# Optimization experiments

Hardware: AMD Instinct MI355X
Metric: run time of the kernel (lower is better)

The kernel has to match this reference:

```python
import jax, jax.numpy as jnp
import numpy as np
import math

B, T = 32768, 34
VOCAB = 14
SQRT_HD = math.sqrt(3.0)

def _pos_flat_index():
    # flatten (source, index) pairs into indices of a [14,3] table:
    # rows 0-9 = digit spiral enc, row 10 = z10_enc, rows 11-13 = special_enc
    flat = []
    for p in range(34):
        if p < 10:
            flat.append(p)
        elif p == 10:
            flat.append(11 + 0)
        elif p < 21:
            flat.append(p - 11)
        elif p == 21:
            flat.append(11 + 1)
        elif p < 33:
            z = p - 22
            flat.append(z if z < 10 else 10)
        else:
            flat.append(11 + 2)
    return np.array(flat, dtype=np.int32)

POS_FLAT = _pos_flat_index()

def setup_inputs() -> dict:
    key = jax.random.key(0)
    ks = jax.random.split(key, 12)
    r = lambda k, s: jax.random.normal(k, s, dtype=jnp.float32)
    return {
        'idx': jax.random.randint(ks[0], (B, T), 0, VOCAB, dtype=jnp.int64),
        'tok_emb': r(ks[1], (14, 3)),
        'pos_params': r(ks[2], (4,)),
        'z10_enc': r(ks[3], (1, 3)),
        'special_enc': r(ks[4], (3, 3)),
        'wq': r(ks[5], (3, 6)), 'wk': r(ks[6], (3, 6)), 'wv': r(ks[7], (3, 6)),
        'wo': r(ks[8], (6, 6)),
        'ln1_g': jnp.ones(6), 'ln1_b': jnp.zeros(6),
        'ln2_g': jnp.ones(6), 'ln2_b': jnp.zeros(6),
        'lnf_g': jnp.ones(6), 'lnf_b': jnp.zeros(6),
        'ffn_w1': r(ks[9], (6, 2)), 'ffn_b1': jnp.zeros(2),
        'ffn_w2': r(ks[10], (2, 6)), 'ffn_b2': jnp.zeros(6),
        'head_w': r(ks[11], (6, 3)),
    }

def _ln(x, g, b):
    mu = x.mean(-1, keepdims=True)
    var = ((x - mu) ** 2).mean(-1, keepdims=True)
    return (x - mu) * jax.lax.rsqrt(var + 1e-5) * g + b

def _forward(idx, tok_emb, pos_params, z10_enc, special_enc, wq, wk, wv, wo,
             ln1_g, ln1_b, ln2_g, ln2_b, lnf_g, lnf_b,
             ffn_w1, ffn_b1, ffn_w2, ffn_b2, head_w):
    amp, phase, slope, offset = pos_params[0], pos_params[1], pos_params[2], pos_params[3]
    i = jnp.arange(10, dtype=jnp.float32)
    ang = 2.0 * math.pi * i / 10.0 + phase
    digit = jnp.stack([amp * jnp.cos(ang), amp * jnp.sin(ang), slope * i + offset], -1)  # [10,3]
    table = jnp.concatenate([digit, z10_enc, special_enc], 0)  # [14,3]
    Tn = idx.shape[1]
    pos = table[POS_FLAT][:Tn]  # [T,3]
    tok = tok_emb[idx]  # [B,T,3]
    x = jnp.concatenate([tok, jnp.broadcast_to(pos, tok.shape)], -1)  # [B,T,6]
    h = _ln(x, ln1_g, ln1_b)
    h_tok, h_pos = h[..., :3], h[..., 3:]
    Bn = idx.shape[0]
    q = (h_pos @ wq).reshape(Bn, Tn, 2, 3)
    k = (h_pos @ wk).reshape(Bn, Tn, 2, 3)
    v = (h_tok @ wv).reshape(Bn, Tn, 2, 3)
    attn = jnp.einsum('bqhd,bkhd->bhqk', q, k) / SQRT_HD
    mask = jnp.tril(jnp.ones((Tn, Tn), bool))
    attn = jax.nn.softmax(jnp.where(mask, attn, -jnp.inf), axis=-1)
    o = jnp.einsum('bhqk,bkhd->bqhd', attn, v).reshape(Bn, Tn, 6)
    x = x + o @ wo
    h2 = _ln(x, ln2_g, ln2_b)
    x = x + (jax.nn.gelu(h2 @ ffn_w1 + ffn_b1, approximate=False) @ ffn_w2 + ffn_b2)
    x = _ln(x, lnf_g, lnf_b)
    return (x @ head_w) @ tok_emb.T  # [B,T,14]

def reference(idx, tok_emb, pos_params, z10_enc, special_enc, wq, wk, wv, wo,
              ln1_g, ln1_b, ln2_g, ln2_b, lnf_g, lnf_b,
              ffn_w1, ffn_b1, ffn_w2, ffn_b2, head_w):
    return _forward(idx, tok_emb, pos_params, z10_enc, special_enc, wq, wk, wv, wo,
                    ln1_g, ln1_b, ln2_g, ln2_b, lnf_g, lnf_b,
                    ffn_w1, ffn_b1, ffn_w2, ffn_b2, head_w)
```

## Files before the change

### kernel.cpp

```cpp
#include <hip/hip_runtime.h>
#include <math.h>

#define BT    34
#define TPR   17
#define RPB   15
#define BLOCK 256

typedef float v4f __attribute__((ext_vector_type(4)));

__device__ __forceinline__ void ln6(const float* x, const float* g, const float* b, float* o) {
  float mu = (x[0]+x[1]+x[2]+x[3]+x[4]+x[5]) * (1.0f/6.0f);
  float v = 0.f;
  #pragma unroll
  for (int c = 0; c < 6; ++c) { float d = x[c]-mu; v += d*d; }
  float inv = rsqrtf(v * (1.0f/6.0f) + 1e-5f);
  #pragma unroll
  for (int c = 0; c < 6; ++c) o[c] = (x[c]-mu)*inv*g[c] + b[c];
}

__global__ __launch_bounds__(BLOCK, 4)
void addtrans_kernel(const int* __restrict__ idx,
                     const float* __restrict__ tok_emb,
                     const float* __restrict__ pos_params,
                     const float* __restrict__ z10_enc,
                     const float* __restrict__ special_enc,
                     const float* __restrict__ wq,
                     const float* __restrict__ wk,
                     const float* __restrict__ wv,
                     const float* __restrict__ wo,
                     const float* __restrict__ ln1_g, const float* __restrict__ ln1_b,
                     const float* __restrict__ ln2_g, const float* __restrict__ ln2_b,
                     const float* __restrict__ lnf_g, const float* __restrict__ lnf_b,
                     const float* __restrict__ ffn_w1, const float* __restrict__ ffn_b1,
                     const float* __restrict__ ffn_w2, const float* __restrict__ ffn_b2,
                     const float* __restrict__ head_w,
                     float* __restrict__ out, int B)
{
  __shared__ __align__(16) float s_mem[RPB*BT*14];
  __shared__ float s_te[42];
  __shared__ float s_pos[BT*3];
  __shared__ float s_wq[18], s_wk[18], s_wv[18], s_wo[36], s_hw[18];
  __shared__ float s_g1[6], s_b1[6], s_g2[6], s_b2[6], s_gf[6], s_bf[6];
  __shared__ float s_w1[12], s_w2[12], s_fb1[2], s_fb2[6];

  const int tid = threadIdx.x;

  if (tid < 42) s_te[tid] = tok_emb[tid];
  if (tid < 18) { s_wq[tid]=wq[tid]; s_wk[tid]=wk[tid]; s_wv[tid]=wv[tid]; s_hw[tid]=head_w[tid]; }
  if (tid < 36) s_wo[tid] = wo[tid];
  if (tid < 12) { s_w1[tid]=ffn_w1[tid]; s_w2[tid]=ffn_w2[tid]; }
  if (tid < 6)  { s_g1[tid]=ln1_g[tid]; s_b1[tid]=ln1_b[tid];
                  s_g2[tid]=ln2_g[tid]; s_b2[tid]=ln2_b[tid];
                  s_gf[tid]=lnf_g[tid]; s_bf[tid]=lnf_b[tid];
                  s_fb2[tid]=ffn_b2[tid]; }
  if (tid < 2)  s_fb1[tid] = ffn_b1[tid];
  if (tid < BT) {
    int p = tid, f;
    if (p < 10) f = p;
    else if (p == 10) f = 11;
    else if (p < 21) f = p - 11;
    else if (p == 21) f = 12;
    else if (p < 33) { int z = p - 22; f = (z < 10) ? z : 10; }
    else f = 13;
    float e0, e1, e2;
    if (f < 10) {
      float amp = pos_params[0], ph = pos_params[1], sl = pos_params[2], of = pos_params[3];
      float ang = 0.62831853071795864769f * (float)f + ph;
      e0 = amp * cosf(ang); e1 = amp * sinf(ang); e2 = sl * (float)f + of;
    } else if (f == 10) { e0 = z10_enc[0]; e1 = z10_enc[1]; e2 = z10_enc[2]; }
    else { int u = f - 11; e0 = special_enc[u*3]; e1 = special_enc[u*3+1]; e2 = special_enc[u*3+2]; }
    s_pos[tid*3+0] = e0; s_pos[tid*3+1] = e1; s_pos[tid*3+2] = e2;
  }
  __syncthreads();

  const int row = tid / TPR;
  const int j   = tid - row * TPR;
  const int b   = blockIdx.x * RPB + row;
  const bool active = (row < RPB) && (b < B);

  float q[2][6], xr[2][6];

  if (active) {
    const int base = b * BT;
    #pragma unroll
    for (int s = 0; s < 2; ++s) {
      const int t = j + s * TPR;
      const int vid = idx[base + t];
      float x6[6];
      x6[0] = s_te[vid*3+0]; x6[1] = s_te[vid*3+1]; x6[2] = s_te[vid*3+2];
      x6[3] = s_pos[t*3+0];  x6[4] = s_pos[t*3+1];  x6[5] = s_pos[t*3+2];
      float h[6];
      ln6(x6, s_g1, s_b1, h);
      float* kvp = &s_mem[(row*BT + t)*12];
      #pragma unroll
      for (int c = 0; c < 6; ++c) {
        q[s][c] = 0.57735026918962576451f *
                  (h[3]*s_wq[c] + h[4]*s_wq[6+c] + h[5]*s_wq[12+c]);
        kvp[c]   = h[3]*s_wk[c] + h[4]*s_wk[6+c] + h[5]*s_wk[12+c];
        kvp[6+c] = h[0]*s_wv[c] + h[1]*s_wv[6+c] + h[2]*s_wv[12+c];
        xr[s][c] = x6[c];
      }
    }
  }
  __syncthreads();

  float l[2][2] = {{0.f,0.f},{0.f,0.f}};
  float o[2][6] = {{0.f,0.f,0.f,0.f,0.f,0.f},{0.f,0.f,0.f,0.f,0.f,0.f}};
  if (active) {
    const float* kvb = &s_mem[row * (BT*12)];
    #pragma unroll 2
    for (int k = 0; k < TPR; ++k) {
      float4 A  = *(const float4*)(kvb + k*12 + 0);
      float4 Bv = *(const float4*)(kvb + k*12 + 4);
      float4 C  = *(const float4*)(kvb + k*12 + 8);
      float sa = q[0][0]*A.x + q[0][1]*A.y + q[0][2]*A.z;
      float sb = q[0][3]*A.w + q[0][4]*Bv.x + q[0][5]*Bv.y;
      float pa = __expf(sa), pb = __expf(sb);
      const bool m = (k <= j);
      pa = m ? pa : 0.f; pb = m ? pb : 0.f;
      l[0][0] += pa; l[0][1] += pb;
      o[0][0] += pa*Bv.z; o[0][1] += pa*Bv.w; o[0][2] += pa*C.x;
      o[0][3] += pb*C.y;  o[0][4] += pb*C.z;  o[0][5] += pb*C.w;
      float sc = q[1][0]*A.x + q[1][1]*A.y + q[1][2]*A.z;
      float sd = q[1][3]*A.w + q[1][4]*Bv.x + q[1][5]*Bv.y;
      float pc = __expf(sc), pd = __expf(sd);
      l[1][0] += pc; l[1][1] += pd;
      o[1][0] += pc*Bv.z; o[1][1] += pc*Bv.w; o[1][2] += pc*C.x;
      o[1][3] += pd*C.y;  o[1][4] += pd*C.z;  o[1][5] += pd*C.w;
    }
    #pragma unroll 2
    for (int k = TPR; k < BT; ++k) {
      float4 A  = *(const float4*)(kvb + k*12 + 0);
      float4 Bv = *(const float4*)(kvb + k*12 + 4);
      float4 C  = *(const float4*)(kvb + k*12 + 8);
      float sc = q[1][0]*A.x + q[1][1]*A.y + q[1][2]*A.z;
      float sd = q[1][3]*A.w + q[1][4]*Bv.x + q[1][5]*Bv.y;
      float pc = __expf(sc), pd = __expf(sd);
      const bool m = (k <= j + TPR);
      pc = m ? pc : 0.f; pd = m ? pd : 0.f;
      l[1][0] += pc; l[1][1] += pd;
      o[1][0] += pc*Bv.z; o[1][1] += pc*Bv.w; o[1][2] += pc*C.x;
      o[1][3] += pd*C.y;  o[1][4] += pd*C.z;  o[1][5] += pd*C.w;
    }
  }
  __syncthreads();

  if (active) {
    #pragma unroll
    for (int s = 0; s < 2; ++s) {
      const int t = j + s * TPR;
      const float ia = 1.0f / l[s][0], ib = 1.0f / l[s][1];
      float a6[6] = { o[s][0]*ia, o[s][1]*ia, o[s][2]*ia,
                      o[s][3]*ib, o[s][4]*ib, o[s][5]*ib };
      float xn[6];
      #pragma unroll
      for (int c = 0; c < 6; ++c) {
        xn[c] = xr[s][c]
              + a6[0]*s_wo[c]    + a6[1]*s_wo[6+c]  + a6[2]*s_wo[12+c]
              + a6[3]*s_wo[18+c] + a6[4]*s_wo[24+c] + a6[5]*s_wo[30+c];
      }
      float h2[6];
      ln6(xn, s_g2, s_b2, h2);
      float a0 = s_fb1[0], a1 = s_fb1[1];
      #pragma unroll
      for (int d = 0; d < 6; ++d) { a0 += h2[d]*s_w1[d*2]; a1 += h2[d]*s_w1[d*2+1]; }
      const float g0 = 0.5f*a0*(1.0f + erff(a0*0.70710678118654752440f));
      const float g1 = 0.5f*a1*(1.0f + erff(a1*0.70710678118654752440f));
      #pragma unroll
      for (int c = 0; c < 6; ++c) xn[c] += g0*s_w2[c] + g1*s_w2[6+c] + s_fb2[c];
      float xf[6];
      ln6(xn, s_gf, s_bf, xf);
      float y0 = 0.f, y1 = 0.f, y2 = 0.f;
      #pragma unroll
      for (int c = 0; c < 6; ++c) {
        y0 += xf[c]*s_hw[c*3+0]; y1 += xf[c]*s_hw[c*3+1]; y2 += xf[c]*s_hw[c*3+2];
      }
      float* lp = &s_mem[(row*BT + t)*14];
      #pragma unroll
      for (int j2 = 0; j2 < 14; ++j2)
        lp[j2] = y0*s_te[j2*3+0] + y1*s_te[j2*3+1] + y2*s_te[j2*3+2];
    }
  }
  __syncthreads();

  {
    const int b0 = blockIdx.x * RPB;
    int nrows = B - b0; if (nrows > RPB) nrows = RPB;
    if (nrows > 0) {
      const int n4 = nrows * (BT*14/4);
      v4f* dst = reinterpret_cast<v4f*>(out + (size_t)b0 * (BT*14));
      const v4f* src = reinterpret_cast<const v4f*>(s_mem);
      for (int i = tid; i < n4; i += BLOCK)
        __builtin_nontemporal_store(src[i], dst + i);
    }
  }
}

extern "C" void kernel_launch(void* const* d_in, const int* in_sizes, int n_in,
                              void* d_out, int out_size, void* d_ws, size_t ws_size,
                              hipStream_t stream) {
  const int B = in_sizes[0] / BT;
  const int grid = (B + RPB - 1) / RPB;
  addtrans_kernel<<<grid, BLOCK, 0, stream>>>(
      (const int*)d_in[0],   (const float*)d_in[1], (const float*)d_in[2],
      (const float*)d_in[3], (const float*)d_in[4], (const float*)d_in[5],
      (const float*)d_in[6], (const float*)d_in[7], (const float*)d_in[8],
      (const float*)d_in[9], (const float*)d_in[10], (const float*)d_in[11],
      (const float*)d_in[12], (const float*)d_in[13], (const float*)d_in[14],
      (const float*)d_in[15], (const float*)d_in[16], (const float*)d_in[17],
      (const float*)d_in[18], (const float*)d_in[19],
      (float*)d_out, B);
}
```

Before: 145.4 us.

## Pack attention math into float2 ops, use exp2, and store outputs directly

```diff
diff --git a/kernel.cpp b/kernel.cpp
--- a/kernel.cpp
+++ b/kernel.cpp
@@ -6,7 +6,16 @@
 #define RPB   15
 #define BLOCK 256
 
+typedef float v2f __attribute__((ext_vector_type(2)));
 typedef float v4f __attribute__((ext_vector_type(4)));
+
+#define QSCALE 0.83294037332470f
+
+#if __has_builtin(__builtin_amdgcn_exp2f)
+#define EXP2(x) __builtin_amdgcn_exp2f(x)
+#else
+#define EXP2(x) exp2f(x)
+#endif
 
 __device__ __forceinline__ void ln6(const float* x, const float* g, const float* b, float* o) {
   float mu = (x[0]+x[1]+x[2]+x[3]+x[4]+x[5]) * (1.0f/6.0f);
@@ -36,7 +45,7 @@
                      const float* __restrict__ head_w,
                      float* __restrict__ out, int B)
 {
-  __shared__ __align__(16) float s_mem[RPB*BT*14];
+  __shared__ __align__(16) float s_kv[RPB*BT*12];
   __shared__ float s_te[42];
   __shared__ float s_pos[BT*3];
   __shared__ float s_wq[18], s_wk[18], s_wv[18], s_wo[36], s_hw[18];
@@ -78,7 +87,8 @@
   const int b   = blockIdx.x * RPB + row;
   const bool active = (row < RPB) && (b < B);
 
-  float q[2][6], xr[2][6];
+  v2f   qp[2][3];
+  float xr[2][6];
 
   if (active) {
     const int base = b * BT;
@@ -91,67 +101,67 @@
       x6[3] = s_pos[t*3+0];  x6[4] = s_pos[t*3+1];  x6[5] = s_pos[t*3+2];
       float h[6];
       ln6(x6, s_g1, s_b1, h);
-      float* kvp = &s_mem[(row*BT + t)*12];
+      float q6[6], k6[6], v6[6];
       #pragma unroll
       for (int c = 0; c < 6; ++c) {
-        q[s][c] = 0.57735026918962576451f *
-                  (h[3]*s_wq[c] + h[4]*s_wq[6+c] + h[5]*s_wq[12+c]);
-        kvp[c]   = h[3]*s_wk[c] + h[4]*s_wk[6+c] + h[5]*s_wk[12+c];
-        kvp[6+c] = h[0]*s_wv[c] + h[1]*s_wv[6+c] + h[2]*s_wv[12+c];
+        q6[c] = h[3]*s_wq[c] + h[4]*s_wq[6+c] + h[5]*s_wq[12+c];
+        k6[c] = h[3]*s_wk[c] + h[4]*s_wk[6+c] + h[5]*s_wk[12+c];
+        v6[c] = h[0]*s_wv[c] + h[1]*s_wv[6+c] + h[2]*s_wv[12+c];
         xr[s][c] = x6[c];
       }
+      qp[s][0] = (v2f){q6[0]*QSCALE, q6[3]*QSCALE};
+      qp[s][1] = (v2f){q6[1]*QSCALE, q6[4]*QSCALE};
+      qp[s][2] = (v2f){q6[2]*QSCALE, q6[5]*QSCALE};
+      v4f* kvp = (v4f*)&s_kv[(row*BT + t)*12];
+      kvp[0] = (v4f){k6[0], k6[3], k6[1], k6[4]};
+      kvp[1] = (v4f){k6[2], k6[5], v6[0], v6[3]};
+      kvp[2] = (v4f){v6[1], v6[4], v6[2], v6[5]};
     }
   }
   __syncthreads();
 
-  float l[2][2] = {{0.f,0.f},{0.f,0.f}};
-  float o[2][6] = {{0.f,0.f,0.f,0.f,0.f,0.f},{0.f,0.f,0.f,0.f,0.f,0.f}};
+  v2f l0 = (v2f){0.f,0.f}, l1 = (v2f){0.f,0.f};
+  v2f o0[3] = {(v2f){0.f,0.f},(v2f){0.f,0.f},(v2f){0.f,0.f}};
+  v2f o1[3] = {(v2f){0.f,0.f},(v2f){0.f,0.f},(v2f){0.f,0.f}};
   if (active) {
-    const float* kvb = &s_mem[row * (BT*12)];
-    #pragma unroll 2
+    const v4f* kvb = (const v4f*)&s_kv[row * (BT*12)];
+    #pragma unroll 4
     for (int k = 0; k < TPR; ++k) {
-      float4 A  = *(const float4*)(kvb + k*12 + 0);
-      float4 Bv = *(const float4*)(kvb + k*12 + 4);
-      float4 C  = *(const float4*)(kvb + k*12 + 8);
-      float sa = q[0][0]*A.x + q[0][1]*A.y + q[0][2]*A.z;
-      float sb = q[0][3]*A.w + q[0][4]*Bv.x + q[0][5]*Bv.y;
-      float pa = __expf(sa), pb = __expf(sb);
-      const bool m = (k <= j);
-      pa = m ? pa : 0.f; pb = m ? pb : 0.f;
-      l[0][0] += pa; l[0][1] += pb;
-      o[0][0] += pa*Bv.z; o[0][1] += pa*Bv.w; o[0][2] += pa*C.x;
-      o[0][3] += pb*C.y;  o[0][4] += pb*C.z;  o[0][5] += pb*C.w;
-      float sc = q[1][0]*A.x + q[1][1]*A.y + q[1][2]*A.z;
-      float sd = q[1][3]*A.w + q[1][4]*Bv.x + q[1][5]*Bv.y;
-      float pc = __expf(sc), pd = __expf(sd);
-      l[1][0] += pc; l[1][1] += pd;
-      o[1][0] += pc*Bv.z; o[1][1] += pc*Bv.w; o[1][2] += pc*C.x;
-      o[1][3] += pd*C.y;  o[1][4] += pd*C.z;  o[1][5] += pd*C.w;
-    }
-    #pragma unroll 2
+      v4f A = kvb[k*3+0], Bv = kvb[k*3+1], C = kvb[k*3+2];
+      v2f kA = (v2f){A.x, A.y}, kB = (v2f){A.z, A.w}, kC = (v2f){Bv.x, Bv.y};
+      v2f vA = (v2f){Bv.z, Bv.w}, vB = (v2f){C.x, C.y}, vC = (v2f){C.z, C.w};
+      v2f s0 = qp[0][0]*kA + qp[0][1]*kB + qp[0][2]*kC;
+      const float mf = (k <= j) ? 1.f : 0.f;
+      v2f p0 = (v2f){EXP2(s0.x), EXP2(s0.y)};
+      p0 *= mf;
+      l0 += p0; o0[0] += p0*vA; o0[1] += p0*vB; o0[2] += p0*vC;
+      v2f s1 = qp[1][0]*kA + qp[1][1]*kB + qp[1][2]*kC;
+      v2f p1 = (v2f){EXP2(s1.x), EXP2(s1.y)};
+      l1 += p1; o1[0] += p1*vA; o1[1] += p1*vB; o1[2] += p1*vC;
+    }
+    #pragma unroll 4
     for (int k = TPR; k < BT; ++k) {
-      float4 A  = *(const float4*)(kvb + k*12 + 0);
-      float4 Bv = *(const float4*)(kvb + k*12 + 4);
-      float4 C  = *(const float4*)(kvb + k*12 + 8);
-      float sc = q[1][0]*A.x + q[1][1]*A.y + q[1][2]*A.z;
-      float sd = q[1][3]*A.w + q[1][4]*Bv.x + q[1][5]*Bv.y;
-      float pc = __expf(sc), pd = __expf(sd);
-      const bool m = (k <= j + TPR);
-      pc = m ? pc : 0.f; pd = m ? pd : 0.f;
-      l[1][0] += pc; l[1][1] += pd;
-      o[1][0] += pc*Bv.z; o[1][1] += pc*Bv.w; o[1][2] += pc*C.x;
-      o[1][3] += pd*C.y;  o[1][4] += pd*C.z;  o[1][5] += pd*C.w;
-    }
-  }
-  __syncthreads();
+      v4f A = kvb[k*3+0], Bv = kvb[k*3+1], C = kvb[k*3+2];
+      v2f kA = (v2f){A.x, A.y}, kB = (v2f){A.z, A.w}, kC = (v2f){Bv.x, Bv.y};
+      v2f vA = (v2f){Bv.z, Bv.w}, vB = (v2f){C.x, C.y}, vC = (v2f){C.z, C.w};
+      v2f s1 = qp[1][0]*kA + qp[1][1]*kB + qp[1][2]*kC;
+      const float mf = (k <= j + TPR) ? 1.f : 0.f;
+      v2f p1 = (v2f){EXP2(s1.x), EXP2(s1.y)};
+      p1 *= mf;
+      l1 += p1; o1[0] += p1*vA; o1[1] += p1*vB; o1[2] += p1*vC;
+    }
+  }
 
   if (active) {
     #pragma unroll
     for (int s = 0; s < 2; ++s) {
       const int t = j + s * TPR;
-      const float ia = 1.0f / l[s][0], ib = 1.0f / l[s][1];
-      float a6[6] = { o[s][0]*ia, o[s][1]*ia, o[s][2]*ia,
-                      o[s][3]*ib, o[s][4]*ib, o[s][5]*ib };
+      const v2f  lv = s ? l1 : l0;
+      const v2f* ov = s ? o1 : o0;
+      const float ia = __builtin_amdgcn_rcpf(lv.x);
+      const float ib = __builtin_amdgcn_rcpf(lv.y);
+      float a6[6] = { ov[0].x*ia, ov[1].x*ia, ov[2].x*ia,
+                      ov[0].y*ib, ov[1].y*ib, ov[2].y*ib };
       float xn[6];
       #pragma unroll
       for (int c = 0; c < 6; ++c) {
@@ -175,23 +185,14 @@
       for (int c = 0; c < 6; ++c) {
         y0 += xf[c]*s_hw[c*3+0]; y1 += xf[c]*s_hw[c*3+1]; y2 += xf[c]*s_hw[c*3+2];
       }
-      float* lp = &s_mem[(row*BT + t)*14];
+      float lg[14];
       #pragma unroll
       for (int j2 = 0; j2 < 14; ++j2)
-        lp[j2] = y0*s_te[j2*3+0] + y1*s_te[j2*3+1] + y2*s_te[j2*3+2];
-    }
-  }
-  __syncthreads();
-
-  {
-    const int b0 = blockIdx.x * RPB;
-    int nrows = B - b0; if (nrows > RPB) nrows = RPB;
-    if (nrows > 0) {
-      const int n4 = nrows * (BT*14/4);
-      v4f* dst = reinterpret_cast<v4f*>(out + (size_t)b0 * (BT*14));
-      const v4f* src = reinterpret_cast<const v4f*>(s_mem);
-      for (int i = tid; i < n4; i += BLOCK)
-        __builtin_nontemporal_store(src[i], dst + i);
+        lg[j2] = y0*s_te[j2*3+0] + y1*s_te[j2*3+1] + y2*s_te[j2*3+2];
+      v2f* op2 = (v2f*)(out + ((size_t)b * BT + t) * 14);
+      #pragma unroll
+      for (int u = 0; u < 7; ++u)
+        op2[u] = (v2f){lg[2*u], lg[2*u+1]};
     }
   }
 }
```

New measurement: 147.2 us. About the same (+1.2%).
